# Optimization experiments

Hardware: AMD Instinct MI355X
Metric: run time of the kernel (lower is better)

## Reference

```python
import jax, jax.numpy as jnp
import numpy as np

N = 10000; E = 320000; B = 262144
F_NODE = 64; F_EDGE = 8; H = 4; C = 32
EVO_IN = C * 4 * H + 1      # 513
EVO_HID = 256; EVO_DIM = 64
FLOW_IN = EVO_DIM + 5       # 69
FLOW_HID = 256
SLOPE = 0.01                # torch LeakyReLU default slope
GAT_SLOPE = 0.2             # GATv2 attention LeakyReLU slope
EPS = 1e-5                  # BatchNorm eps


def setup_inputs() -> dict:
    key = jax.random.key(0)
    ks = iter(jax.random.split(key, 64))
    def nrm(shape, scale=1.0):
        return jax.random.normal(next(ks), shape, jnp.float32) * scale
    inp = {}
    inp['x1'] = nrm((N, F_NODE))
    inp['edge_index1'] = jax.random.randint(next(ks), (2, E), 0, N)
    inp['edge_attr1'] = nrm((E, F_EDGE))
    inp['x2'] = nrm((N, F_NODE))
    inp['edge_index2'] = jax.random.randint(next(ks), (2, E), 0, N)
    inp['edge_attr2'] = nrm((E, F_EDGE))
    inp['dist_m'] = jax.random.uniform(next(ks), (N, N), jnp.float32)
    inp['node_visit'] = jax.random.uniform(next(ks), (N, 2), jnp.float32)
    inp['od_nodes'] = jax.random.randint(next(ks), (B, 2), 0, N)
    # GATv2Conv params per snapshot: lin_l, lin_r (bias=True), lin_edge (bias=False), att [H,C], out bias [H*C]
    for p in ('g1', 'g2'):
        s = 1.0 / np.sqrt(F_NODE)
        inp[p + '_Wl'] = nrm((H * C, F_NODE), s)
        inp[p + '_bl'] = jnp.zeros((H * C,), jnp.float32)
        inp[p + '_Wr'] = nrm((H * C, F_NODE), s)
        inp[p + '_br'] = jnp.zeros((H * C,), jnp.float32)
        inp[p + '_We'] = nrm((H * C, F_EDGE), 1.0 / np.sqrt(F_EDGE))
        inp[p + '_att'] = nrm((H, C), 1.0 / np.sqrt(C))
        inp[p + '_bias'] = jnp.zeros((H * C,), jnp.float32)
    # EvoEmbedding (all Linear bias=False)
    inp['e_W1'] = nrm((EVO_HID, EVO_IN), 1.0 / np.sqrt(EVO_IN))
    inp['e_W2'] = nrm((EVO_HID, EVO_HID), 1.0 / np.sqrt(EVO_HID))
    inp['e_W3'] = nrm((EVO_HID, EVO_HID), 1.0 / np.sqrt(EVO_HID))
    inp['e_W4'] = nrm((EVO_HID // 2, EVO_HID), 1.0 / np.sqrt(EVO_HID))
    inp['e_Wout'] = nrm((EVO_DIM, EVO_HID // 2), 1.0 / np.sqrt(EVO_HID // 2))
    # FlowGenerator (Linear bias=False) + BatchNorm affine params
    inp['f_W1'] = nrm((FLOW_HID, FLOW_IN), 1.0 / np.sqrt(FLOW_IN))
    inp['f_W2'] = nrm((FLOW_HID, FLOW_HID), 1.0 / np.sqrt(FLOW_HID))
    inp['f_W3'] = nrm((FLOW_HID, FLOW_HID), 1.0 / np.sqrt(FLOW_HID))
    inp['f_W4'] = nrm((FLOW_HID // 2, FLOW_HID), 1.0 / np.sqrt(FLOW_HID))
    inp['f_Wout'] = nrm((1, FLOW_HID // 2), 1.0 / np.sqrt(FLOW_HID // 2))
    inp['f_g1'] = jnp.ones((FLOW_HID,), jnp.float32);  inp['f_b1'] = jnp.zeros((FLOW_HID,), jnp.float32)
    inp['f_g2'] = jnp.ones((FLOW_HID,), jnp.float32);  inp['f_b2'] = jnp.zeros((FLOW_HID,), jnp.float32)
    inp['f_g3'] = jnp.ones((FLOW_HID,), jnp.float32);  inp['f_b3'] = jnp.zeros((FLOW_HID,), jnp.float32)
    inp['f_g4'] = jnp.ones((FLOW_HID // 2,), jnp.float32); inp['f_b4'] = jnp.zeros((FLOW_HID // 2,), jnp.float32)
    return inp


def _gatv2(x, ei, ea, Wl, bl, Wr, br, We, att, bias):
    src, dst = ei[0], ei[1]
    # self-loops with fill_value='mean': per-target mean of incoming edge_attr
    deg = jax.ops.segment_sum(jnp.ones_like(dst, jnp.float32), dst, N)
    mean_attr = jax.ops.segment_sum(ea, dst, N) / jnp.maximum(deg, 1.0)[:, None]
    loops = jnp.arange(N)
    s = jnp.concatenate([src, loops]); d = jnp.concatenate([dst, loops])
    eaf = jnp.concatenate([ea, mean_attr], axis=0)            # [E+N, F_EDGE]
    xl = (x @ Wl.T + bl).reshape(N, H, C)                     # source transform
    xr = (x @ Wr.T + br).reshape(N, H, C)                     # target transform
    em = (eaf @ We.T).reshape(-1, H, C)
    msg = jax.nn.leaky_relu(xl[s] + xr[d] + em, GAT_SLOPE)    # [E+N, H, C]
    scr = jnp.einsum('ehc,hc->eh', msg, att)                  # [E+N, H]
    mx = jax.ops.segment_max(scr, d, N)
    ex = jnp.exp(scr - mx[d])
    den = jax.ops.segment_sum(ex, d, N)
    alpha = ex / den[d]                                       # softmax over incoming edges
    out = jax.ops.segment_sum(alpha[:, :, None] * xl[s], d, N).reshape(N, H * C) + bias
    return jax.nn.relu(out), alpha


def _evo(v, W1, W2, W3, W4, Wout):
    h = jax.nn.leaky_relu(v @ W1.T, SLOPE)
    h = jax.nn.leaky_relu(h @ W2.T, SLOPE)
    h = jax.nn.leaky_relu(h @ W3.T, SLOPE)
    h = jax.nn.leaky_relu(h @ W4.T, SLOPE)
    return h @ Wout.T


def _bn(x, g, b):
    mu = x.mean(0)
    var = x.var(0)
    return (x - mu) * jax.lax.rsqrt(var + EPS) * g + b


def _flow(v, W1, W2, W3, W4, Wout, g1, b1, g2, b2, g3, b3, g4, b4):
    h = jax.nn.leaky_relu(_bn(v @ W1.T, g1, b1), SLOPE)
    h = jax.nn.leaky_relu(_bn(h @ W2.T, g2, b2), SLOPE)
    h = jax.nn.leaky_relu(_bn(h @ W3.T, g3, b3), SLOPE)
    h = jax.nn.leaky_relu(_bn(h @ W4.T, g4, b4), SLOPE)
    return (h @ Wout.T).squeeze(-1)


def reference(x1, edge_index1, edge_attr1, x2, edge_index2, edge_attr2, dist_m, node_visit, od_nodes,
              g1_Wl, g1_bl, g1_Wr, g1_br, g1_We, g1_att, g1_bias,
              g2_Wl, g2_bl, g2_Wr, g2_br, g2_We, g2_att, g2_bias,
              e_W1, e_W2, e_W3, e_W4, e_Wout,
              f_W1, f_W2, f_W3, f_W4, f_Wout,
              f_g1, f_b1, f_g2, f_b2, f_g3, f_b3, f_g4, f_b4):
    n1, a1 = _gatv2(x1, edge_index1, edge_attr1, g1_Wl, g1_bl, g1_Wr, g1_br, g1_We, g1_att, g1_bias)
    n2, a2 = _gatv2(x2, edge_index2, edge_attr2, g2_Wl, g2_bl, g2_Wr, g2_br, g2_We, g2_att, g2_bias)
    o = od_nodes[:, 0]; dn = od_nodes[:, 1]
    dist = dist_m[o, dn][:, None]                              # fused gather replacing python loop
    feat = jnp.concatenate([n1[o], n1[dn], n2[o], n2[dn], dist], axis=1)  # [B, 513]
    evo = _evo(feat, e_W1, e_W2, e_W3, e_W4, e_Wout)           # [B, EVO_DIM]
    # NOTE: original uses node_visit[:,0] for BOTH o_visit and d_visit (kept faithful)
    ov = node_visit[o, 0:1]; dv = node_visit[dn, 0:1]
    ovn = node_visit[o, 1:2]; dvn = node_visit[dn, 1:2]
    cat = jnp.concatenate([evo, ov, dv, ovn, dvn, dist], axis=1)  # [B, 69]
    inferred = _flow(cat, f_W1, f_W2, f_W3, f_W4, f_Wout, f_g1, f_b1, f_g2, f_b2, f_g3, f_b3, f_g4, f_b4)
    return (inferred, a1, a2, evo)
```

## Files before the change

### kernel.cpp

```cpp
#include <hip/hip_runtime.h>

typedef unsigned short u16;
typedef unsigned int u32;

#define NN 10000
#define NE 320000
#define ET 330000
#define NB 262144

typedef __attribute__((ext_vector_type(8))) short bf16x8;
typedef __attribute__((ext_vector_type(4))) float f32x4;

__device__ __forceinline__ u16 f2b(float f) {
  u32 u = __float_as_uint(f);
  u += 0x7fffu + ((u >> 16) & 1u);
  return (u16)(u >> 16);
}
__device__ __forceinline__ float b2f(u16 h) {
  return __uint_as_float(((u32)h) << 16);
}
__device__ __forceinline__ float lrelu(float v, float s) { return v > 0.f ? v : v * s; }

__device__ __forceinline__ void g2lds16(const void* g, void* l) {
  __builtin_amdgcn_global_load_lds((const __attribute__((address_space(1))) void*)g,
                                   (__attribute__((address_space(3))) void*)l, 16, 0, 0);
}

__global__ __launch_bounds__(256) void k_prep(const float* __restrict__ eW2, const float* __restrict__ eW3,
                                              const float* __restrict__ eW4, const float* __restrict__ eWo,
                                              const float* __restrict__ fW1, const float* __restrict__ fW2,
                                              const float* __restrict__ fW3, const float* __restrict__ fW4,
                                              const float* __restrict__ eW1,
                                              u16* eW2b, u16* eW3b, u16* eW4b, u16* eWob,
                                              u16* fW2b, u16* fW3b, u16* fW4b,
                                              float* W1T, float* w512, u16* combW) {
  const int blk = blockIdx.x, tid = threadIdx.x;
  if (blk < 256) {
    int t = blk * 256 + tid; eW2b[t] = f2b(eW2[t]);
  } else if (blk < 512) {
    int t = (blk - 256) * 256 + tid; eW3b[t] = f2b(eW3[t]);
  } else if (blk < 640) {
    int t = (blk - 512) * 256 + tid; eW4b[t] = f2b(eW4[t]);
  } else if (blk < 672) {
    int t = (blk - 640) * 256 + tid; eWob[t] = f2b(eWo[t]);
  } else if (blk < 928) {
    int t = (blk - 672) * 256 + tid; fW2b[t] = f2b(fW2[t]);
  } else if (blk < 1184) {
    int t = (blk - 928) * 256 + tid; fW3b[t] = f2b(fW3[t]);
  } else if (blk < 1312) {
    int t = (blk - 1184) * 256 + tid; fW4b[t] = f2b(fW4[t]);
  } else if (blk < 1568) {
    int m = blk - 1312;
    for (int k = tid; k < 512; k += 256) W1T[(size_t)k * 256 + m] = eW1[(size_t)m * 513 + k];
  } else if (blk == 1568) {
    w512[tid] = eW1[(size_t)tid * 513 + 512];
  } else {
    int m = blk - 1569;
    int k = tid;
    if (k < 160) {
      float v = 0.f;
      if (k < 128) {
        const float* fr = fW1 + (size_t)m * 69;
        for (int j = 0; j < 64; ++j) v += fr[j] * eWo[(size_t)j * 128 + k];
      } else if (k < 133) {
        v = fW1[(size_t)m * 69 + 64 + (k - 128)];
      }
      combW[(size_t)m * 160 + k] = f2b(v);
    }
  }
}

__global__ __launch_bounds__(256) void k_sprep(const int* __restrict__ od, const float* __restrict__ dm,
                                               const float* __restrict__ nv,
                                               float* __restrict__ distb, u16* __restrict__ bufC) {
  int b = blockIdx.x * 256 + threadIdx.x;
  int o = od[b * 2], d = od[b * 2 + 1];
  float dist = dm[(size_t)o * NN + d];
  distb[b] = dist;
  u16 tmp[32];
  tmp[0] = f2b(nv[o * 2]);
  tmp[1] = f2b(nv[d * 2]);
  tmp[2] = f2b(nv[o * 2 + 1]);
  tmp[3] = f2b(nv[d * 2 + 1]);
  tmp[4] = f2b(dist);
#pragma unroll
  for (int k = 5; k < 32; ++k) tmp[k] = 0;
  u16* p = bufC + (size_t)b * 160 + 128;
#pragma unroll
  for (int k = 0; k < 4; ++k) *(bf16x8*)(p + k * 8) = *(bf16x8*)(tmp + k * 8);
}

__global__ __launch_bounds__(256) void k_count(const int* __restrict__ ei, int* __restrict__ cnt) {
  int t = blockIdx.x * 256 + threadIdx.x;
  if (t >= ET) return;
  int d = (t < NE) ? ei[NE + t] : (t - NE);
  atomicAdd(&cnt[d], 1);
}

__global__ __launch_bounds__(1024) void k_scan(const int* __restrict__ cnt, int* __restrict__ cs) {
  __shared__ int part[1024];
  int tid = threadIdx.x;
  int base = tid * 10;
  int local[10];
  int s = 0;
#pragma unroll
  for (int i = 0; i < 10; ++i) {
    int idx = base + i;
    int v = (idx < NN) ? cnt[idx] : 0;
    local[i] = s; s += v;
  }
  part[tid] = s;
  __syncthreads();
  for (int off = 1; off < 1024; off <<= 1) {
    int v = (tid >= off) ? part[tid - off] : 0;
    __syncthreads();
    part[tid] += v;
    __syncthreads();
  }
  int pre = (tid > 0) ? part[tid - 1] : 0;
#pragma unroll
  for (int i = 0; i < 10; ++i) {
    int idx = base + i;
    if (idx < NN) cs[idx] = pre + local[i];
  }
  if (tid == 1023) cs[NN] = part[1023];
}

__global__ __launch_bounds__(256) void k_fill(const int* __restrict__ ei, const int* __restrict__ cs,
                                              int* __restrict__ wr, int2* __restrict__ csr) {
  int t = blockIdx.x * 256 + threadIdx.x;
  if (t >= ET) return;
  int s, d;
  if (t < NE) { s = ei[t]; d = ei[NE + t]; } else { s = t - NE; d = s; }
  int pos = atomicAdd(&wr[d], 1);
  csr[cs[d] + pos] = make_int2(t, s);
}

__global__ __launch_bounds__(256) void k_asum(const int2* __restrict__ csr, const int* __restrict__ cs,
                                              const float* __restrict__ ea, float* __restrict__ asum) {
  int wid = (blockIdx.x * 256 + threadIdx.x) >> 6;
  int lane = threadIdx.x & 63;
  int beg = cs[wid], end = cs[wid + 1];
  int j = lane & 7, slot = lane >> 3;
  float acc = 0.f;
  for (int i = beg + slot; i < end; i += 8) {
    int e = csr[i].x;
    if (e < NE) acc += ea[(size_t)e * 8 + j];
  }
  acc += __shfl_xor(acc, 8);
  acc += __shfl_xor(acc, 16);
  acc += __shfl_xor(acc, 32);
  if (lane < 8) {
    float dr = (float)(end - beg - 1);
    asum[(size_t)wid * 8 + lane] = acc / fmaxf(dr, 1.f);
  }
}

__global__ __launch_bounds__(256) void k_xlr(const float* __restrict__ x,
                                             const float* __restrict__ Wl, const float* __restrict__ bl,
                                             const float* __restrict__ Wr, const float* __restrict__ br,
                                             float* __restrict__ xl, float* __restrict__ xr) {
  __shared__ float sx[128];
  int nb = blockIdx.x * 2;
  for (int i = threadIdx.x; i < 128; i += 256) sx[i] = x[(size_t)nb * 64 + i];
  __syncthreads();
  int half = threadIdx.x >> 7;
  int node = nb + half;
  int m = threadIdx.x & 127;
  const float* xv = sx + (half << 6);
  float al = bl[m], ar = br[m];
  const float* wl = Wl + (size_t)m * 64;
  const float* wr = Wr + (size_t)m * 64;
#pragma unroll 8
  for (int k = 0; k < 64; ++k) { float xk = xv[k]; al += xk * wl[k]; ar += xk * wr[k]; }
  xl[(size_t)node * 128 + m] = al;
  xr[(size_t)node * 128 + m] = ar;
}

__global__ __launch_bounds__(256) void k_scr(const float* __restrict__ xl, const float* __restrict__ xr,
                                             const int* __restrict__ ei, const float* __restrict__ ea,
                                             const float* __restrict__ mattr,
                                             const float* __restrict__ We, const float* __restrict__ att,
                                             float* __restrict__ scr) {
  const int lane = threadIdx.x & 63;
  const int sub = lane & 31;
  const int half = lane >> 5;
  float4 w0[4], w1[4];
#pragma unroll
  for (int c = 0; c < 4; ++c) {
    const float* wp = We + (size_t)(sub * 4 + c) * 8;
    w0[c] = *(const float4*)wp;
    w1[c] = *(const float4*)(wp + 4);
  }
  const float4 attv = *(const float4*)(att + sub * 4);
  const int gw = (blockIdx.x * 256 + threadIdx.x) >> 6;
  const int nw = gridDim.x * 4;
  for (int p = gw; p < ET / 2; p += nw) {
    int e = p * 2 + half;
    int s, d; const float* ap;
    if (e < NE) { s = ei[e]; d = ei[NE + e]; ap = ea + (size_t)e * 8; }
    else { s = e - NE; d = s; ap = mattr + (size_t)(e - NE) * 8; }
    float4 a0 = *(const float4*)ap;
    float4 a1 = *(const float4*)(ap + 4);
    float4 xlv = *(const float4*)(xl + (size_t)s * 128 + sub * 4);
    float4 xrv = *(const float4*)(xr + (size_t)d * 128 + sub * 4);
    const float* xle = (const float*)&xlv;
    const float* xre = (const float*)&xrv;
    const float* ate = (const float*)&attv;
    float psum = 0.f;
#pragma unroll
    for (int c = 0; c < 4; ++c) {
      float em = a0.x * w0[c].x + a0.y * w0[c].y + a0.z * w0[c].z + a0.w * w0[c].w
               + a1.x * w1[c].x + a1.y * w1[c].y + a1.z * w1[c].z + a1.w * w1[c].w;
      float v = xle[c] + xre[c] + em;
      v = v > 0.f ? v : 0.2f * v;
      psum += v * ate[c];
    }
    psum += __shfl_xor(psum, 1);
    psum += __shfl_xor(psum, 2);
    psum += __shfl_xor(psum, 4);
    if ((sub & 7) == 0) scr[(size_t)e * 4 + (sub >> 3)] = psum;
  }
}

__global__ __launch_bounds__(256) void k_nodered(const float* __restrict__ scr, const int2* __restrict__ csr,
                                                 const int* __restrict__ cs, const float* __restrict__ xl,
                                                 const float* __restrict__ bias,
                                                 float* __restrict__ m_out, float* __restrict__ den_out,
                                                 float* __restrict__ nout) {
  int d = (blockIdx.x * 256 + threadIdx.x) >> 6;
  int lane = threadIdx.x & 63;
  int h0 = lane >> 5;
  int beg = cs[d], end = cs[d + 1];
  float mx0 = -3.4e38f, mx1 = -3.4e38f;
  for (int i = beg; i < end; ++i) {
    int e = csr[i].x;
    mx0 = fmaxf(mx0, scr[(size_t)e * 4 + h0]);
    mx1 = fmaxf(mx1, scr[(size_t)e * 4 + h0 + 2]);
  }
  float acc0 = 0.f, acc1 = 0.f, dn0 = 0.f, dn1 = 0.f;
  for (int i = beg; i < end; ++i) {
    int2 es = csr[i];
    float ex0 = __expf(scr[(size_t)es.x * 4 + h0] - mx0);
    float ex1 = __expf(scr[(size_t)es.x * 4 + h0 + 2] - mx1);
    dn0 += ex0; dn1 += ex1;
    const float* xp = xl + (size_t)es.y * 128;
    acc0 += ex0 * xp[lane];
    acc1 += ex1 * xp[64 + lane];
  }
  if (lane == 0 || lane == 32) {
    m_out[d * 4 + h0] = mx0;     m_out[d * 4 + h0 + 2] = mx1;
    den_out[d * 4 + h0] = dn0;   den_out[d * 4 + h0 + 2] = dn1;
  }
  nout[(size_t)d * 128 + lane] = fmaxf(acc0 / dn0 + bias[lane], 0.f);
  nout[(size_t)d * 128 + 64 + lane] = fmaxf(acc1 / dn1 + bias[64 + lane], 0.f);
}

__global__ __launch_bounds__(256) void k_alpha(const float* __restrict__ scr, const int* __restrict__ ei,
                                               const float* __restrict__ m, const float* __restrict__ den,
                                               float* __restrict__ aout) {
  int t = blockIdx.x * 256 + threadIdx.x;
  if (t >= ET * 4) return;
  int e = t >> 2, h = t & 3;
  int d = (e < NE) ? ei[NE + e] : (e - NE);
  aout[t] = __expf(scr[t] - m[d * 4 + h]) / den[d * 4 + h];
}

__global__ __launch_bounds__(256) void k_qtab(const float* __restrict__ n1, const float* __restrict__ n2,
                                              const float* __restrict__ W1T,
                                              u16* __restrict__ Qo, u16* __restrict__ Qd) {
  __shared__ float s1[2048], s2[2048];
  int nb = blockIdx.x * 16;
  for (int i = threadIdx.x; i < 2048; i += 256) {
    s1[i] = n1[(size_t)nb * 128 + i];
    s2[i] = n2[(size_t)nb * 128 + i];
  }
  __syncthreads();
  int m = threadIdx.x;
  float qo[16], qd[16];
#pragma unroll
  for (int i = 0; i < 16; ++i) { qo[i] = 0.f; qd[i] = 0.f; }
#pragma unroll 2
  for (int k = 0; k < 128; ++k) {
    float w0 = W1T[(size_t)k * 256 + m];
    float w1 = W1T[(size_t)(128 + k) * 256 + m];
    float w2 = W1T[(size_t)(256 + k) * 256 + m];
    float w3 = W1T[(size_t)(384 + k) * 256 + m];
#pragma unroll
    for (int i = 0; i < 16; ++i) {
      float a = s1[i * 128 + k], b = s2[i * 128 + k];
      qo[i] += a * w0 + b * w2;
      qd[i] += a * w1 + b * w3;
    }
  }
#pragma unroll
  for (int i = 0; i < 16; ++i) {
    Qo[(size_t)(nb + i) * 256 + m] = f2b(qo[i]);
    Qd[(size_t)(nb + i) * 256 + m] = f2b(qd[i]);
  }
}

__global__ __launch_bounds__(256) void k_evo1(const u16* __restrict__ Qo, const u16* __restrict__ Qd,
                                              const int* __restrict__ od, const float* __restrict__ distb,
                                              const float* __restrict__ w512, u16* __restrict__ h1) {
  __shared__ float sw[256];
  sw[threadIdx.x] = w512[threadIdx.x];
  __syncthreads();
  int t = blockIdx.x * 256 + threadIdx.x;
  int b = t >> 5, mq = (t & 31) << 3;
  int o = od[b * 2], d = od[b * 2 + 1];
  float dist = distb[b];
  bf16x8 qa = *(const bf16x8*)(Qo + (size_t)o * 256 + mq);
  bf16x8 qc = *(const bf16x8*)(Qd + (size_t)d * 256 + mq);
  bf16x8 r;
#pragma unroll
  for (int j = 0; j < 8; ++j) {
    float v = b2f((u16)qa[j]) + b2f((u16)qc[j]) + dist * sw[mq + j];
    r[j] = (short)f2b(lrelu(v, 0.01f));
  }
  *(bf16x8*)(h1 + (size_t)b * 256 + mq) = r;
}

template <int NF, int EPI, int BNA>
__global__ __launch_bounds__(512) void gemm256(const u16* __restrict__ A, const u16* __restrict__ W,
                                               int K, size_t lda,
                                               u16* __restrict__ obf, int ld_bf,
                                               float* __restrict__ stats,
                                               const float* __restrict__ stin, const float* __restrict__ gg,
                                               const float* __restrict__ bb, float invB) {
  constexpr int M = NF * 64;
  constexpr int CPW = 2 + NF / 2;
  __shared__ alignas(16) u16 Alds[2][256 * 32];
  __shared__ alignas(16) u16 Blds[2][M * 32];
  __shared__ float sS[256], sT[256];
  const int tid = threadIdx.x;
  const int lane = tid & 63;
  const int w = tid >> 6;
  const int wr = w >> 2, wc = w & 3;
  const size_t rowBase = (size_t)blockIdx.x * 256;

  if (BNA) {
    for (int c = tid; c < K; c += 512) {
      float mu = stin[c] * invB;
      float var = stin[K + c] * invB - mu * mu;
      float sc = rsqrtf(var + 1e-5f) * gg[c];
      sS[c] = sc;
      sT[c] = bb[c] - mu * sc;
    }
    __syncthreads();
  }

  f32x4 acc[8][NF];
  const f32x4 z4 = {0.f, 0.f, 0.f, 0.f};
#pragma unroll
  for (int m = 0; m < 8; ++m)
#pragma unroll
    for (int n = 0; n < NF; ++n) acc[m][n] = z4;

  const int crow = lane >> 2;
  const int ccol = (lane & 3) << 3;
  const int KT = K >> 5;

  auto stage = [&](int buf, int kb) {
#pragma unroll
    for (int i = 0; i < CPW; ++i) {
      const int c = w * CPW + i;
      if (c < 16) {
        const u16* src = A + (rowBase + (c << 4) + crow) * lda + kb + ccol;
        g2lds16(src, &Alds[buf][(c << 4) << 5]);
      } else {
        const u16* src = W + (size_t)(((c - 16) << 4) + crow) * K + kb + ccol;
        g2lds16(src, &Blds[buf][((c - 16) << 4) << 5]);
      }
    }
  };

  stage(0, 0);
  int cur = 0;
  const int lr = lane & 15, lk = (lane >> 4) << 3;
  for (int kt = 0; kt < KT; ++kt) {
    const int kb = kt << 5;
    if (kt + 1 < KT) {
      stage(cur ^ 1, kb + 32);
      if constexpr (NF == 4)
        asm volatile("s_waitcnt vmcnt(4)" ::: "memory");
      else
        asm volatile("s_waitcnt vmcnt(3)" ::: "memory");
    } else {
      asm volatile("s_waitcnt vmcnt(0)" ::: "memory");
    }
    __builtin_amdgcn_s_barrier();

    float sv[8], tv[8];
    if (BNA) {
      float4 s0 = *(const float4*)&sS[kb + lk];
      float4 s1 = *(const float4*)&sS[kb + lk + 4];
      float4 t0 = *(const float4*)&sT[kb + lk];
      float4 t1 = *(const float4*)&sT[kb + lk + 4];
      sv[0] = s0.x; sv[1] = s0.y; sv[2] = s0.z; sv[3] = s0.w;
      sv[4] = s1.x; sv[5] = s1.y; sv[6] = s1.z; sv[7] = s1.w;
      tv[0] = t0.x; tv[1] = t0.y; tv[2] = t0.z; tv[3] = t0.w;
      tv[4] = t1.x; tv[5] = t1.y; tv[6] = t1.z; tv[7] = t1.w;
    }
    bf16x8 bfr[NF];
#pragma unroll
    for (int n = 0; n < NF; ++n)
      bfr[n] = *(const bf16x8*)&Blds[cur][((((wc * NF + n) << 4) + lr) << 5) + lk];
#pragma unroll
    for (int m = 0; m < 8; ++m) {
      bf16x8 af = *(const bf16x8*)&Alds[cur][(((wr << 7) + (m << 4) + lr) << 5) + lk];
      if (BNA) {
        bf16x8 o;
#pragma unroll
        for (int j = 0; j < 8; ++j) {
          float v = fmaf(b2f((u16)af[j]), sv[j], tv[j]);
          v = v > 0.f ? v : v * 0.01f;
          o[j] = (short)f2b(v);
        }
        af = o;
      }
#pragma unroll
      for (int n = 0; n < NF; ++n)
        acc[m][n] = __builtin_amdgcn_mfma_f32_16x16x32_bf16(af, bfr[n], acc[m][n], 0, 0, 0);
    }
    __builtin_amdgcn_s_barrier();
    cur ^= 1;
  }

  const int lg = lane >> 4;
  float csm[NF], cq[NF];
#pragma unroll
  for (int n = 0; n < NF; ++n) { csm[n] = 0.f; cq[n] = 0.f; }
#pragma unroll
  for (int m = 0; m < 8; ++m) {
#pragma unroll
    for (int n = 0; n < NF; ++n) {
      const int col = wc * (NF * 16) + (n << 4) + lr;
#pragma unroll
      for (int j = 0; j < 4; ++j) {
        const size_t row = rowBase + (wr << 7) + (m << 4) + (lg << 2) + j;
        float v = acc[m][n][j];
        if (EPI == 0) {
          v = v > 0.f ? v : v * 0.01f;
          obf[row * ld_bf + col] = f2b(v);
        } else {
          obf[row * ld_bf + col] = f2b(v);
          csm[n] += v; cq[n] += v * v;
        }
      }
    }
  }
  if (EPI == 1) {
#pragma unroll
    for (int n = 0; n < NF; ++n) {
      float s = csm[n], q = cq[n];
      s += __shfl_xor(s, 16); s += __shfl_xor(s, 32);
      q += __shfl_xor(q, 16); q += __shfl_xor(q, 32);
      if (lane < 16) {
        const int col = wc * (NF * 16) + (n << 4) + lane;
        atomicAdd(&stats[col], s);
        atomicAdd(&stats[M + col], q);
      }
    }
  }
}

template <int NF>
__global__ __launch_bounds__(256) void gemm_f32out(const u16* __restrict__ A, const u16* __restrict__ W,
                                                   int K, size_t lda, int M, float* __restrict__ of32) {
  constexpr int CW = NF * 16;
  __shared__ alignas(16) u16 Alds[2][128 * 32];
  __shared__ alignas(16) u16 Blds[2][CW * 2 * 32];
  const int lane = threadIdx.x & 63;
  const int w = threadIdx.x >> 6;
  const int wr = w >> 1, wc = w & 1;
  const size_t rowBase = (size_t)blockIdx.x * 128;

  f32x4 acc[4][NF];
  const f32x4 z4 = {0.f, 0.f, 0.f, 0.f};
#pragma unroll
  for (int m = 0; m < 4; ++m)
#pragma unroll
    for (int n = 0; n < NF; ++n) acc[m][n] = z4;

  const int sr = (w << 4) + (lane >> 2);
  const int sc = (lane & 3) << 3;
  const int KT = K >> 5;

  auto stage = [&](int buf, int kb) {
#pragma unroll
    for (int i = 0; i < 2; ++i) {
      const u16* src = A + (rowBase + (i << 6) + sr) * lda + kb + sc;
      g2lds16(src, &Alds[buf][((i << 6) + (w << 4)) << 5]);
    }
#pragma unroll
    for (int i = 0; i < NF / 2; ++i) {
      const u16* src = W + (size_t)((i << 6) + sr) * K + kb + sc;
      g2lds16(src, &Blds[buf][((i << 6) + (w << 4)) << 5]);
    }
  };

  stage(0, 0);
  int cur = 0;
  for (int kt = 0; kt < KT; ++kt) {
    if (kt + 1 < KT) {
      stage(cur ^ 1, (kt + 1) << 5);
      asm volatile("s_waitcnt vmcnt(3)" ::: "memory");
    } else {
      asm volatile("s_waitcnt vmcnt(0)" ::: "memory");
    }
    __builtin_amdgcn_s_barrier();
    const int lr = lane & 15, lk = (lane >> 4) << 3;
    bf16x8 af[4], bfr[NF];
#pragma unroll
    for (int m = 0; m < 4; ++m)
      af[m] = *(const bf16x8*)&Alds[cur][(((wr << 6) + (m << 4) + lr) << 5) + lk];
#pragma unroll
    for (int n = 0; n < NF; ++n)
      bfr[n] = *(const bf16x8*)&Blds[cur][((wc * CW + (n << 4) + lr) << 5) + lk];
#pragma unroll
    for (int m = 0; m < 4; ++m)
#pragma unroll
      for (int n = 0; n < NF; ++n)
        acc[m][n] = __builtin_amdgcn_mfma_f32_16x16x32_bf16(af[m], bfr[n], acc[m][n], 0, 0, 0);
    __builtin_amdgcn_s_barrier();
    cur ^= 1;
  }

  const int lr = lane & 15, lg = lane >> 4;
#pragma unroll
  for (int m = 0; m < 4; ++m) {
#pragma unroll
    for (int n = 0; n < NF; ++n) {
      const int col = wc * CW + (n << 4) + lr;
      if (col >= M) continue;
#pragma unroll
      for (int j = 0; j < 4; ++j) {
        const size_t row = rowBase + (wr << 6) + (m << 4) + (lg << 2) + j;
        of32[row * M + col] = acc[m][n][j];
      }
    }
  }
}

__global__ __launch_bounds__(256) void k_fout4(const u16* __restrict__ pre, const float* __restrict__ st,
                                               const float* __restrict__ g, const float* __restrict__ b,
                                               const float* __restrict__ W, float* __restrict__ out,
                                               float invB) {
  __shared__ float smu[128], srs[128], sg[128], sb[128], sw[128];
  if (threadIdx.x < 128) {
    int c = threadIdx.x;
    float mu = st[c] * invB;
    float var = st[128 + c] * invB - mu * mu;
    smu[c] = mu;
    srs[c] = rsqrtf(var + 1e-5f);
    sg[c] = g[c];
    sb[c] = b[c];
    sw[c] = W[c];
  }
  __syncthreads();
  int bi = blockIdx.x * 256 + threadIdx.x;
  const u16* hp = pre + (size_t)bi * 128;
  float acc = 0.f;
#pragma unroll
  for (int k = 0; k < 128; k += 8) {
    bf16x8 u = *(const bf16x8*)(hp + k);
#pragma unroll
    for (int j = 0; j < 8; ++j) {
      int c = k + j;
      float v = (b2f((u16)u[j]) - smu[c]) * srs[c] * sg[c] + sb[c];
      v = b2f(f2b(lrelu(v, 0.01f)));
      acc += v * sw[c];
    }
  }
  out[bi] = acc;
}

extern "C" void kernel_launch(void* const* d_in, const int* in_sizes, int n_in,
                              void* d_out, int out_size, void* d_ws, size_t ws_size,
                              hipStream_t stream) {
  (void)in_sizes; (void)n_in; (void)out_size; (void)ws_size;

  const float* x[2] = {(const float*)d_in[0], (const float*)d_in[3]};
  const int* ei[2] = {(const int*)d_in[1], (const int*)d_in[4]};
  const float* ea[2] = {(const float*)d_in[2], (const float*)d_in[5]};
  const float* dm = (const float*)d_in[6];
  const float* nv = (const float*)d_in[7];
  const int* od = (const int*)d_in[8];
  const float* Wl[2] = {(const float*)d_in[9], (const float*)d_in[16]};
  const float* bl[2] = {(const float*)d_in[10], (const float*)d_in[17]};
  const float* Wr[2] = {(const float*)d_in[11], (const float*)d_in[18]};
  const float* br[2] = {(const float*)d_in[12], (const float*)d_in[19]};
  const float* We[2] = {(const float*)d_in[13], (const float*)d_in[20]};
  const float* att[2] = {(const float*)d_in[14], (const float*)d_in[21]};
  const float* bia[2] = {(const float*)d_in[15], (const float*)d_in[22]};
  const float* eW1 = (const float*)d_in[23];
  const float* eW2 = (const float*)d_in[24];
  const float* eW3 = (const float*)d_in[25];
  const float* eW4 = (const float*)d_in[26];
  const float* eWo = (const float*)d_in[27];
  const float* fW1 = (const float*)d_in[28];
  const float* fW2 = (const float*)d_in[29];
  const float* fW3 = (const float*)d_in[30];
  const float* fW4 = (const float*)d_in[31];
  const float* fWo = (const float*)d_in[32];
  const float* fg[4] = {(const float*)d_in[33], (const float*)d_in[35], (const float*)d_in[37], (const float*)d_in[39]};
  const float* fb[4] = {(const float*)d_in[34], (const float*)d_in[36], (const float*)d_in[38], (const float*)d_in[40]};

  float* out_inf = (float*)d_out;
  float* out_a1 = out_inf + NB;
  float* out_a2 = out_a1 + (size_t)ET * 4;
  float* out_evo = out_a2 + (size_t)ET * 4;

  char* base = (char*)d_ws;
  size_t cur = 0;
  auto carve = [&](size_t bytes) -> char* {
    char* p = base + cur;
    cur += (bytes + 255) & ~(size_t)255;
    return p;
  };
  u16* bufA = (u16*)carve((size_t)NB * 256 * 2);
  u16* bufB = (u16*)carve((size_t)NB * 256 * 2);
  u16* bufC = (u16*)carve((size_t)NB * 160 * 2);
  float* n1 = (float*)carve((size_t)NN * 128 * 4);
  float* n2 = (float*)carve((size_t)NN * 128 * 4);
  u16* Qob = (u16*)carve((size_t)NN * 256 * 2);
  u16* Qdb = (u16*)carve((size_t)NN * 256 * 2);
  float* xl = (float*)carve((size_t)NN * 128 * 4);
  float* xr = (float*)carve((size_t)NN * 128 * 4);
  int* cnt = (int*)carve((size_t)(NN + 1) * 4);
  int* wr = (int*)carve((size_t)NN * 4);
  int* cs = (int*)carve((size_t)(NN + 1) * 4);
  int2* csr = (int2*)carve((size_t)ET * 8);
  float* m_out = (float*)carve((size_t)NN * 4 * 4);
  float* den_out = (float*)carve((size_t)NN * 4 * 4);
  float* asum = (float*)carve((size_t)NN * 8 * 4);
  float* scr = (float*)carve((size_t)ET * 4 * 4);
  float* distb = (float*)carve((size_t)NB * 4);
  float* w512 = (float*)carve(1024);
  float* W1T = (float*)carve(512 * 256 * 4);
  float* stats = (float*)carve(1792 * 4);
  float* st[4] = {stats, stats + 512, stats + 1024, stats + 1536};
  u16* eW2b = (u16*)carve(256 * 256 * 2);
  u16* eW3b = (u16*)carve(256 * 256 * 2);
  u16* eW4b = (u16*)carve(128 * 256 * 2);
  u16* eWob = (u16*)carve(64 * 128 * 2);
  u16* fW2b = (u16*)carve(256 * 256 * 2);
  u16* fW3b = (u16*)carve(256 * 256 * 2);
  u16* fW4b = (u16*)carve(128 * 256 * 2);
  u16* combW = (u16*)carve(256 * 160 * 2);

  k_prep<<<1825, 256, 0, stream>>>(eW2, eW3, eW4, eWo, fW1, fW2, fW3, fW4, eW1,
                                   eW2b, eW3b, eW4b, eWob, fW2b, fW3b, fW4b,
                                   W1T, w512, combW);
  hipMemsetAsync(stats, 0, 1792 * 4, stream);
  k_sprep<<<NB / 256, 256, 0, stream>>>(od, dm, nv, distb, bufC);

  float* nout[2] = {n1, n2};
  float* aout[2] = {out_a1, out_a2};
  const int EB = (ET + 255) / 256;
  const size_t cwSpan = (size_t)((char*)wr - (char*)cnt) + (size_t)NN * 4;
  for (int gi = 0; gi < 2; ++gi) {
    hipMemsetAsync(cnt, 0, cwSpan, stream);
    k_count<<<EB, 256, 0, stream>>>(ei[gi], cnt);
    k_scan<<<1, 1024, 0, stream>>>(cnt, cs);
    k_fill<<<EB, 256, 0, stream>>>(ei[gi], cs, wr, csr);
    k_asum<<<NN / 4, 256, 0, stream>>>(csr, cs, ea[gi], asum);
    k_xlr<<<NN / 2, 256, 0, stream>>>(x[gi], Wl[gi], bl[gi], Wr[gi], br[gi], xl, xr);
    k_scr<<<2048, 256, 0, stream>>>(xl, xr, ei[gi], ea[gi], asum, We[gi], att[gi], scr);
    k_nodered<<<NN / 4, 256, 0, stream>>>(scr, csr, cs, xl, bia[gi], m_out, den_out, nout[gi]);
    k_alpha<<<(ET * 4 + 255) / 256, 256, 0, stream>>>(scr, ei[gi], m_out, den_out, aout[gi]);
  }

  k_qtab<<<NN / 16, 256, 0, stream>>>(n1, n2, W1T, Qob, Qdb);
  k_evo1<<<NB * 32 / 256, 256, 0, stream>>>(Qob, Qdb, od, distb, w512, bufA);

  const float invB = 1.0f / (float)NB;
  const int GB = NB / 256;
  gemm256<4, 0, 0><<<GB, 512, 0, stream>>>(bufA, eW2b, 256, 256, bufB, 256, nullptr, nullptr, nullptr, nullptr, 0.f);
  gemm256<4, 0, 0><<<GB, 512, 0, stream>>>(bufB, eW3b, 256, 256, bufA, 256, nullptr, nullptr, nullptr, nullptr, 0.f);
  gemm256<2, 0, 0><<<GB, 512, 0, stream>>>(bufA, eW4b, 256, 256, bufC, 160, nullptr, nullptr, nullptr, nullptr, 0.f);
  gemm_f32out<2><<<NB / 128, 256, 0, stream>>>(bufC, eWob, 128, 160, 64, out_evo);

  gemm256<4, 1, 0><<<GB, 512, 0, stream>>>(bufC, combW, 160, 160, bufA, 256, st[0], nullptr, nullptr, nullptr, 0.f);
  gemm256<4, 1, 1><<<GB, 512, 0, stream>>>(bufA, fW2b, 256, 256, bufB, 256, st[1], st[0], fg[0], fb[0], invB);
  gemm256<4, 1, 1><<<GB, 512, 0, stream>>>(bufB, fW3b, 256, 256, bufA, 256, st[2], st[1], fg[1], fb[1], invB);
  gemm256<2, 1, 1><<<GB, 512, 0, stream>>>(bufA, fW4b, 256, 256, bufB, 128, st[3], st[2], fg[2], fb[2], invB);
  k_fout4<<<NB / 256, 256, 0, stream>>>(bufB, st[3], fg[3], fb[3], fWo, out_inf, invB);
}
```

Before: 1.389 ms.

## Fuse evo layer-1 gather and activation into first evo GEMM A-operand staging

Removes the standalone k_evo1 kernel, which gathered Qo/Qd rows per OD pair, added the dist term, applied LeakyReLU and wrote a B×256 bf16 hidden buffer. The new gemm256_evo kernel computes the same values on the fly while staging the A tile into LDS, software-pipelined two k-steps ahead with manual vmcnt waits. This avoids writing and re-reading the 256-wide hidden activation for all B rows, and saves a launch. In exchange, the A loads become random row gathers inside the GEMM, the k-loop has more complex manual synchronisation, and register pressure rises from the prefetched A registers.

Measured after the change: 1.386 ms. Within noise of the previous version (-0.2%).

```diff
diff --git a/kernel.cpp b/kernel.cpp
--- a/kernel.cpp
+++ b/kernel.cpp
@@ -25,6 +25,18 @@
   __builtin_amdgcn_global_load_lds((const __attribute__((address_space(1))) void*)g,
                                    (__attribute__((address_space(3))) void*)l, 16, 0, 0);
 }
+
+template <int N> __device__ __forceinline__ void waitv() {
+  if constexpr (N == 0) asm volatile("s_waitcnt vmcnt(0)" ::: "memory");
+  else if constexpr (N == 1) asm volatile("s_waitcnt vmcnt(1)" ::: "memory");
+  else if constexpr (N == 2) asm volatile("s_waitcnt vmcnt(2)" ::: "memory");
+  else if constexpr (N == 3) asm volatile("s_waitcnt vmcnt(3)" ::: "memory");
+  else if constexpr (N == 4) asm volatile("s_waitcnt vmcnt(4)" ::: "memory");
+  else if constexpr (N == 5) asm volatile("s_waitcnt vmcnt(5)" ::: "memory");
+  else asm volatile("s_waitcnt vmcnt(6)" ::: "memory");
+}
+__device__ __forceinline__ void waitl0() { asm volatile("s_waitcnt lgkmcnt(0)" ::: "memory"); }
+__device__ __forceinline__ void fence() { asm volatile("" ::: "memory"); }
 
 __global__ __launch_bounds__(256) void k_prep(const float* __restrict__ eW2, const float* __restrict__ eW3,
                                               const float* __restrict__ eW4, const float* __restrict__ eWo,
@@ -300,27 +312,6 @@
   }
 }
 
-__global__ __launch_bounds__(256) void k_evo1(const u16* __restrict__ Qo, const u16* __restrict__ Qd,
-                                              const int* __restrict__ od, const float* __restrict__ distb,
-                                              const float* __restrict__ w512, u16* __restrict__ h1) {
-  __shared__ float sw[256];
-  sw[threadIdx.x] = w512[threadIdx.x];
-  __syncthreads();
-  int t = blockIdx.x * 256 + threadIdx.x;
-  int b = t >> 5, mq = (t & 31) << 3;
-  int o = od[b * 2], d = od[b * 2 + 1];
-  float dist = distb[b];
-  bf16x8 qa = *(const bf16x8*)(Qo + (size_t)o * 256 + mq);
-  bf16x8 qc = *(const bf16x8*)(Qd + (size_t)d * 256 + mq);
-  bf16x8 r;
-#pragma unroll
-  for (int j = 0; j < 8; ++j) {
-    float v = b2f((u16)qa[j]) + b2f((u16)qc[j]) + dist * sw[mq + j];
-    r[j] = (short)f2b(lrelu(v, 0.01f));
-  }
-  *(bf16x8*)(h1 + (size_t)b * 256 + mq) = r;
-}
-
 template <int NF, int EPI, int BNA>
 __global__ __launch_bounds__(512) void gemm256(const u16* __restrict__ A, const u16* __restrict__ W,
                                                int K, size_t lda,
@@ -377,7 +368,7 @@
 
   stage(0, 0);
   int cur = 0;
-  const int lr = lane & 15, lk = (lane >> 4) << 3;
+  const int lr = lane & 15, lk = (lane >> 4) << 3, lg = lane >> 4;
   for (int kt = 0; kt < KT; ++kt) {
     const int kb = kt << 5;
     if (kt + 1 < KT) {
@@ -427,7 +418,6 @@
     cur ^= 1;
   }
 
-  const int lg = lane >> 4;
   float csm[NF], cq[NF];
 #pragma unroll
   for (int n = 0; n < NF; ++n) { csm[n] = 0.f; cq[n] = 0.f; }
@@ -460,6 +450,130 @@
         const int col = wc * (NF * 16) + (n << 4) + lane;
         atomicAdd(&stats[col], s);
         atomicAdd(&stats[M + col], q);
+      }
+    }
+  }
+}
+
+__global__ __launch_bounds__(512) void gemm256_evo(const u16* __restrict__ W,
+                                                   u16* __restrict__ obf,
+                                                   const u16* __restrict__ Qo, const u16* __restrict__ Qd,
+                                                   const int* __restrict__ od, const float* __restrict__ distb,
+                                                   const float* __restrict__ w512) {
+  constexpr int KT = 8;
+  __shared__ alignas(16) u16 Alds[2][256 * 32];
+  __shared__ alignas(16) u16 Blds[2][256 * 32];
+  __shared__ float sW[256], sDist[256];
+  __shared__ int sO[256], sD[256];
+  const int tid = threadIdx.x;
+  const int lane = tid & 63;
+  const int w = tid >> 6;
+  const int wr = w >> 2, wc = w & 3;
+  const size_t rowBase = (size_t)blockIdx.x * 256;
+  const int crow = lane >> 2, ccol = (lane & 3) << 3;
+  const int arow = tid >> 1;
+  const int acol = (tid & 1) << 4;
+  const int lr = lane & 15, lk = (lane >> 4) << 3, lg = lane >> 4;
+
+  if (tid < 256) {
+    int2 p = ((const int2*)od)[rowBase + tid];
+    sO[tid] = p.x; sD[tid] = p.y;
+    sDist[tid] = distb[rowBase + tid];
+    sW[tid] = w512[tid];
+  }
+  __syncthreads();
+
+  auto stageB = [&](int buf, int kb) {
+#pragma unroll
+    for (int i = 0; i < 2; ++i) {
+      int c = w * 2 + i;
+      const u16* src = W + (size_t)((c << 4) + crow) * 256 + kb + ccol;
+      g2lds16(src, &Blds[buf][(c << 4) << 5]);
+    }
+  };
+  auto loadA = [&](int kb, bf16x8& r0, bf16x8& r1, bf16x8& r2, bf16x8& r3) {
+    const u16* qo = Qo + (size_t)sO[arow] * 256 + kb + acol;
+    const u16* qd = Qd + (size_t)sD[arow] * 256 + kb + acol;
+    r0 = *(const bf16x8*)qo; r1 = *(const bf16x8*)(qo + 8);
+    r2 = *(const bf16x8*)qd; r3 = *(const bf16x8*)(qd + 8);
+  };
+  auto writeA = [&](int buf, int kb, bf16x8 r0, bf16x8 r1, bf16x8 r2, bf16x8 r3) {
+    float dist = sDist[arow];
+    bf16x8 w0, w1;
+#pragma unroll
+    for (int j = 0; j < 8; ++j) {
+      float v = b2f((u16)r0[j]) + b2f((u16)r2[j]) + dist * sW[kb + acol + j];
+      w0[j] = (short)f2b(lrelu(v, 0.01f));
+      float v2 = b2f((u16)r1[j]) + b2f((u16)r3[j]) + dist * sW[kb + acol + 8 + j];
+      w1[j] = (short)f2b(lrelu(v2, 0.01f));
+    }
+    *(bf16x8*)&Alds[buf][arow * 32 + acol] = w0;
+    *(bf16x8*)&Alds[buf][arow * 32 + acol + 8] = w1;
+  };
+
+  f32x4 acc[8][4];
+  const f32x4 z4 = {0.f, 0.f, 0.f, 0.f};
+#pragma unroll
+  for (int m = 0; m < 8; ++m)
+#pragma unroll
+    for (int n = 0; n < 4; ++n) acc[m][n] = z4;
+
+  bf16x8 p0, p1, p2, p3;
+  {
+    bf16x8 c0, c1, c2, c3;
+    loadA(0, c0, c1, c2, c3);
+    writeA(0, 0, c0, c1, c2, c3);
+  }
+  stageB(0, 0);
+  fence();
+  loadA(32, p0, p1, p2, p3);
+  fence();
+  waitv<4>();
+  waitl0();
+  __builtin_amdgcn_s_barrier();
+
+  int cur = 0;
+  for (int kt = 0; kt < KT; ++kt) {
+    const int kb = kt << 5;
+    const bool hasN = kt + 1 < KT, hasNN = kt + 2 < KT;
+    bf16x8 bfr[4];
+#pragma unroll
+    for (int n = 0; n < 4; ++n)
+      bfr[n] = *(const bf16x8*)&Blds[cur][((((wc << 2) + n) << 4) + lr) * 32 + lk];
+    if (hasN) stageB(cur ^ 1, kb + 32);
+    fence();
+    bf16x8 q0, q1, q2, q3;
+    if (hasNN) loadA(kb + 64, q0, q1, q2, q3);
+    fence();
+#pragma unroll
+    for (int m = 0; m < 8; ++m) {
+      bf16x8 af = *(const bf16x8*)&Alds[cur][(((wr << 7) + (m << 4) + lr) << 5) + lk];
+#pragma unroll
+      for (int n = 0; n < 4; ++n)
+        acc[m][n] = __builtin_amdgcn_mfma_f32_16x16x32_bf16(af, bfr[n], acc[m][n], 0, 0, 0);
+    }
+    if (hasN) {
+      if (hasNN) waitv<6>(); else waitv<2>();
+      writeA(cur ^ 1, kb + 32, p0, p1, p2, p3);
+      p0 = q0; p1 = q1; p2 = q2; p3 = q3;
+      if (hasNN) waitv<4>(); else waitv<0>();
+      waitl0();
+    }
+    __builtin_amdgcn_s_barrier();
+    cur ^= 1;
+  }
+
+#pragma unroll
+  for (int m = 0; m < 8; ++m) {
+#pragma unroll
+    for (int n = 0; n < 4; ++n) {
+      const int col = (wc << 6) + (n << 4) + lr;
+#pragma unroll
+      for (int j = 0; j < 4; ++j) {
+        const size_t row = rowBase + (wr << 7) + (m << 4) + (lg << 2) + j;
+        float v = acc[m][n][j];
+        v = v > 0.f ? v : v * 0.01f;
+        obf[row * 256 + col] = f2b(v);
       }
     }
   }
@@ -673,18 +787,23 @@
   }
 
   k_qtab<<<NN / 16, 256, 0, stream>>>(n1, n2, W1T, Qob, Qdb);
-  k_evo1<<<NB * 32 / 256, 256, 0, stream>>>(Qob, Qdb, od, distb, w512, bufA);
 
   const float invB = 1.0f / (float)NB;
   const int GB = NB / 256;
-  gemm256<4, 0, 0><<<GB, 512, 0, stream>>>(bufA, eW2b, 256, 256, bufB, 256, nullptr, nullptr, nullptr, nullptr, 0.f);
-  gemm256<4, 0, 0><<<GB, 512, 0, stream>>>(bufB, eW3b, 256, 256, bufA, 256, nullptr, nullptr, nullptr, nullptr, 0.f);
-  gemm256<2, 0, 0><<<GB, 512, 0, stream>>>(bufA, eW4b, 256, 256, bufC, 160, nullptr, nullptr, nullptr, nullptr, 0.f);
+  gemm256_evo<<<GB, 512, 0, stream>>>(eW2b, bufA, Qob, Qdb, od, distb, w512);
+  gemm256<4, 0, 0><<<GB, 512, 0, stream>>>(bufA, eW3b, 256, 256, bufB, 256, nullptr,
+                                           nullptr, nullptr, nullptr, 0.f);
+  gemm256<2, 0, 0><<<GB, 512, 0, stream>>>(bufB, eW4b, 256, 256, bufC, 160, nullptr,
+                                           nullptr, nullptr, nullptr, 0.f);
   gemm_f32out<2><<<NB / 128, 256, 0, stream>>>(bufC, eWob, 128, 160, 64, out_evo);
 
-  gemm256<4, 1, 0><<<GB, 512, 0, stream>>>(bufC, combW, 160, 160, bufA, 256, st[0], nullptr, nullptr, nullptr, 0.f);
-  gemm256<4, 1, 1><<<GB, 512, 0, stream>>>(bufA, fW2b, 256, 256, bufB, 256, st[1], st[0], fg[0], fb[0], invB);
-  gemm256<4, 1, 1><<<GB, 512, 0, stream>>>(bufB, fW3b, 256, 256, bufA, 256, st[2], st[1], fg[1], fb[1], invB);
-  gemm256<2, 1, 1><<<GB, 512, 0, stream>>>(bufA, fW4b, 256, 256, bufB, 128, st[3], st[2], fg[2], fb[2], invB);
+  gemm256<4, 1, 0><<<GB, 512, 0, stream>>>(bufC, combW, 160, 160, bufA, 256, st[0],
+                                           nullptr, nullptr, nullptr, 0.f);
+  gemm256<4, 1, 1><<<GB, 512, 0, stream>>>(bufA, fW2b, 256, 256, bufB, 256, st[1],
+                                           st[0], fg[0], fb[0], invB);
+  gemm256<4, 1, 1><<<GB, 512, 0, stream>>>(bufB, fW3b, 256, 256, bufA, 256, st[2],
+                                           st[1], fg[1], fb[1], invB);
+  gemm256<2, 1, 1><<<GB, 512, 0, stream>>>(bufA, fW4b, 256, 256, bufB, 128, st[3],
+                                           st[2], fg[2], fb[2], invB);
   k_fout4<<<NB / 256, 256, 0, stream>>>(bufB, st[3], fg[3], fb[3], fWo, out_inf, invB);
 }
```
